# Kernel tuning notes

Hardware: AMD Instinct MI355X
Metric: run time of the kernel (lower is better)

The kernel has to match this reference:

```python
import jax, jax.numpy as jnp
import numpy as np

N = 50000      # nodes
E = 800000     # edges (avg degree 16)
G = 256        # graphs in batch
IN = 128       # in_channels
H = 256        # hidden_channels
L = 4          # num_layers


def setup_inputs() -> dict:
    key = jax.random.key(0)
    ks = jax.random.split(key, 16)
    x = jax.random.normal(ks[0], (N, IN), dtype=jnp.float32)
    edge_index = jax.random.randint(ks[1], (2, E), 0, N, dtype=jnp.int64)
    batch = jnp.sort(jax.random.randint(ks[2], (N,), 0, G, dtype=jnp.int64))
    s_in = 1.0 / np.sqrt(IN)
    s_h = 1.0 / np.sqrt(H)
    return {
        "x": x,
        "edge_index": edge_index,
        "batch": batch,
        "w1_0": jax.random.normal(ks[3], (IN, H), jnp.float32) * s_in,
        "b1_0": jnp.zeros((H,), jnp.float32),
        "w2_0": jax.random.normal(ks[4], (H, H), jnp.float32) * s_h,
        "b2_0": jnp.zeros((H,), jnp.float32),
        "w1s": jax.random.normal(ks[5], (L - 1, H, H), jnp.float32) * s_h,
        "b1s": jnp.zeros((L - 1, H), jnp.float32),
        "w2s": jax.random.normal(ks[6], (L - 1, H, H), jnp.float32) * s_h,
        "b2s": jnp.zeros((L - 1, H), jnp.float32),
    }


def reference(x, edge_index, batch, w1_0, b1_0, w2_0, b2_0, w1s, b1s, w2s, b2s):
    n_nodes = x.shape[0]
    src, dst = edge_index[0], edge_index[1]

    def gin_layer(h, w1, b1, w2, b2):
        # scatter-add neighbor aggregation: out[i] = sum_{(j->i)} h[j]
        agg = jax.ops.segment_sum(h[src], dst, num_segments=n_nodes)
        z = h + agg  # GIN with eps = 0: (1+eps)*x + aggr
        z = jax.nn.relu(z @ w1 + b1) @ w2 + b2  # MLP: Linear-ReLU-Linear
        return jax.nn.relu(z)  # outer F.relu in forward

    h = gin_layer(x, w1_0, b1_0, w2_0, b2_0)
    for i in range(L - 1):  # small fixed layer loop
        h = gin_layer(h, w1s[i], b1s[i], w2s[i], b2s[i])

    # global_add_pool: per-graph segment sum -> [G, H]
    return jax.ops.segment_sum(h, batch, num_segments=G)
```

## Files before the change

kernel.cpp:

```cpp
#include <hip/hip_runtime.h>
#include <hip/hip_bf16.h>

#define NN 50000
#define NE 800000
#define NG 256
#define CIN 128
#define CH 256

typedef unsigned short u16;
typedef unsigned int u32;
typedef __attribute__((ext_vector_type(8))) short short8;
typedef __attribute__((ext_vector_type(8))) unsigned short ushort8;
typedef __attribute__((ext_vector_type(4))) float f32x4;

__device__ __forceinline__ float bf2f(u16 u) { return __uint_as_float(((u32)u) << 16); }
__device__ __forceinline__ u16 f2bf(float f) {
    u32 u = __float_as_uint(f);
    return (u16)((u + 0x7fffu + ((u >> 16) & 1u)) >> 16);
}

__global__ void k_prep(const float* __restrict__ x, u16* __restrict__ xb,
                       const float* __restrict__ w1_0, const float* __restrict__ w2_0,
                       const float* __restrict__ w1s, const float* __restrict__ w2s,
                       u16* __restrict__ Wp, int* __restrict__ deg_fill,
                       float* __restrict__ outf) {
    int t = blockIdx.x * 256 + threadIdx.x;
    if (t < 2 * NN) deg_fill[t] = 0;
    if (t < NG * CH) outf[t] = 0.f;
    if (t < NN * CIN / 4) {
        float4 v = ((const float4*)x)[t];
        ushort4 o; o.x = f2bf(v.x); o.y = f2bf(v.y); o.z = f2bf(v.z); o.w = f2bf(v.w);
        ((ushort4*)xb)[t] = o;
    }
    if (t < CIN * CH + 7 * CH * CH) {
        const float* Wsrc; int rem;
        if (t < CIN * CH) { Wsrc = w1_0; rem = t; }
        else {
            int o = t - CIN * CH;
            int m = o >> 16; rem = o & 65535;
            Wsrc = (m == 0) ? w2_0
                 : (m <= 3) ? w1s + (size_t)(m - 1) * 65536
                            : w2s + (size_t)(m - 4) * 65536;
        }
        int j = rem & 7, lane = (rem >> 3) & 63, nt = (rem >> 9) & 15, kb = rem >> 13;
        int k = kb * 32 + ((lane >> 4) << 3) + j;
        int nc = nt * 16 + (lane & 15);
        Wp[t] = f2bf(Wsrc[k * CH + nc]);
    }
}

__global__ void k_count_deg(const int* __restrict__ dst, int* __restrict__ deg) {
    int e = blockIdx.x * 256 + threadIdx.x;
    if (e < NE) atomicAdd(&deg[dst[e]], 1);
}

__global__ void k_scan1(const int* __restrict__ deg, int* __restrict__ bsum) {
    __shared__ int sd[256];
    int base = blockIdx.x * 1024, t = threadIdx.x, s = 0;
    for (int j = 0; j < 4; j++) { int i = base + t * 4 + j; if (i < NN) s += deg[i]; }
    sd[t] = s; __syncthreads();
    for (int off = 128; off > 0; off >>= 1) { if (t < off) sd[t] += sd[t + off]; __syncthreads(); }
    if (t == 0) bsum[blockIdx.x] = sd[0];
}

__global__ void k_scan2(int* bsum, int nb, int* row_ptr) {
    int lane = threadIdx.x;
    int v = (lane < nb) ? bsum[lane] : 0;
    int s = v;
    for (int off = 1; off < 64; off <<= 1) {
        int t = __shfl_up(s, off, 64);
        if (lane >= off) s += t;
    }
    if (lane < nb) bsum[lane] = s - v;
    if (lane == 0) row_ptr[NN] = NE;
}

__global__ void k_scan3(const int* __restrict__ deg, const int* __restrict__ bsum,
                        int* __restrict__ row_ptr) {
    __shared__ int sd[256];
    int base = blockIdx.x * 1024, t = threadIdx.x;
    int v[4]; int s = 0;
    for (int j = 0; j < 4; j++) { int i = base + t * 4 + j; v[j] = (i < NN) ? deg[i] : 0; s += v[j]; }
    sd[t] = s; __syncthreads();
    for (int off = 1; off < 256; off <<= 1) {
        int tmp = (t >= off) ? sd[t - off] : 0; __syncthreads();
        sd[t] += tmp; __syncthreads();
    }
    int run = bsum[blockIdx.x] + sd[t] - s;
    for (int j = 0; j < 4; j++) { int i = base + t * 4 + j; if (i < NN) row_ptr[i] = run; run += v[j]; }
}

__global__ void k_fill(const int* __restrict__ src, const int* __restrict__ dst,
                       const int* __restrict__ row_ptr, int* __restrict__ fill,
                       int* __restrict__ col) {
    int e = blockIdx.x * 256 + threadIdx.x;
    if (e < NE) {
        int d = dst[e];
        int pos = row_ptr[d] + atomicAdd(&fill[d], 1);
        col[pos] = src[e];
    }
}

#define ZS 264
template <int K1, bool POOL>
__global__ __launch_bounds__(256, 8) void k_layer(const u16* __restrict__ G,
                                                  const int* __restrict__ row_ptr,
                                                  const int* __restrict__ col,
                                                  const u16* __restrict__ Wp1,
                                                  const float* __restrict__ b1,
                                                  const u16* __restrict__ Wp2,
                                                  const float* __restrict__ b2,
                                                  u16* __restrict__ out,
                                                  const int* __restrict__ batchp,
                                                  float* __restrict__ outf) {
    __shared__ __align__(16) u16 zs[32 * ZS];
    const int tid = threadIdx.x;
    const int wave = tid >> 6, lane = tid & 63;
    const int quad = lane >> 4, l16 = lane & 15;
    const int m0 = blockIdx.x * 32;

    constexpr int LPR = K1 / 8;
    constexpr int RPG = 64 / LPR;
    const int sub = lane / LPR;
    const int c0 = (lane % LPR) * 8;
    for (int g = 0; g < 8; g += RPG) {
        int lr = wave * 8 + g + sub;
        int r = m0 + lr; if (r >= NN) r = NN - 1;
        const u16* base = G + c0;
        float a[8];
        ushort8 sv = *(const ushort8*)(base + (size_t)r * K1);
#pragma unroll
        for (int i = 0; i < 8; i++) a[i] = bf2f(sv[i]);
        int beg = row_ptr[r], end = row_ptr[r + 1];
        int e = beg;
        for (; e + 8 <= end; e += 8) {
            ushort8 v[8];
#pragma unroll
            for (int q = 0; q < 8; q++)
                v[q] = *(const ushort8*)(base + (size_t)col[e + q] * K1);
#pragma unroll
            for (int q = 0; q < 8; q++)
#pragma unroll
                for (int i = 0; i < 8; i++) a[i] += bf2f(v[q][i]);
        }
        for (; e < end; e++) {
            ushort8 nv = *(const ushort8*)(base + (size_t)col[e] * K1);
#pragma unroll
            for (int i = 0; i < 8; i++) a[i] += bf2f(nv[i]);
        }
        ushort8 o;
#pragma unroll
        for (int i = 0; i < 8; i++) o[i] = f2bf(a[i]);
        *(ushort8*)(zs + lr * ZS + c0) = o;
    }
    __syncthreads();

    f32x4 acc[2][4];
#pragma unroll
    for (int ri = 0; ri < 2; ri++)
#pragma unroll
        for (int nj = 0; nj < 4; nj++) acc[ri][nj] = (f32x4){0.f, 0.f, 0.f, 0.f};

    const u16* w1b = Wp1 + (wave * 4) * 512 + lane * 8;
    const u16* w2b = Wp2 + (wave * 4) * 512 + lane * 8;
    constexpr int KB1 = K1 / 32;
    short8 b_cur[4], b_nxt[4];
#pragma unroll
    for (int nj = 0; nj < 4; nj++) b_cur[nj] = *(const short8*)(w1b + nj * 512);

#pragma unroll
    for (int kb = 0; kb < KB1; kb++) {
        int kn = (kb + 1 < KB1) ? (kb + 1) : kb;
#pragma unroll
        for (int nj = 0; nj < 4; nj++)
            b_nxt[nj] = *(const short8*)(w1b + kn * 8192 + nj * 512);
        short8 a[2];
#pragma unroll
        for (int ri = 0; ri < 2; ri++)
            a[ri] = *(const short8*)(zs + (ri * 16 + l16) * ZS + kb * 32 + quad * 8);
#pragma unroll
        for (int nj = 0; nj < 4; nj++)
#pragma unroll
            for (int ri = 0; ri < 2; ri++)
                acc[ri][nj] = __builtin_amdgcn_mfma_f32_16x16x32_bf16(a[ri], b_cur[nj], acc[ri][nj], 0, 0, 0);
#pragma unroll
        for (int nj = 0; nj < 4; nj++) b_cur[nj] = b_nxt[nj];
    }

    short8 b2_cur[4];
#pragma unroll
    for (int nj = 0; nj < 4; nj++) b2_cur[nj] = *(const short8*)(w2b + nj * 512);

    __syncthreads();

#pragma unroll
    for (int nj = 0; nj < 4; nj++) {
        int cc = wave * 64 + nj * 16 + l16;
        float bv = b1[cc];
#pragma unroll
        for (int ri = 0; ri < 2; ri++) {
            f32x4 v = acc[ri][nj];
#pragma unroll
            for (int j = 0; j < 4; j++)
                zs[(ri * 16 + quad * 4 + j) * ZS + cc] = f2bf(fmaxf(v[j] + bv, 0.f));
        }
    }
    __syncthreads();

#pragma unroll
    for (int ri = 0; ri < 2; ri++)
#pragma unroll
        for (int nj = 0; nj < 4; nj++) acc[ri][nj] = (f32x4){0.f, 0.f, 0.f, 0.f};

#pragma unroll
    for (int kb = 0; kb < 8; kb++) {
        int kn = (kb + 1 < 8) ? (kb + 1) : kb;
#pragma unroll
        for (int nj = 0; nj < 4; nj++)
            b_nxt[nj] = *(const short8*)(w2b + kn * 8192 + nj * 512);
        short8 a[2];
#pragma unroll
        for (int ri = 0; ri < 2; ri++)
            a[ri] = *(const short8*)(zs + (ri * 16 + l16) * ZS + kb * 32 + quad * 8);
#pragma unroll
        for (int nj = 0; nj < 4; nj++)
#pragma unroll
            for (int ri = 0; ri < 2; ri++)
                acc[ri][nj] = __builtin_amdgcn_mfma_f32_16x16x32_bf16(a[ri], b2_cur[nj], acc[ri][nj], 0, 0, 0);
#pragma unroll
        for (int nj = 0; nj < 4; nj++) b2_cur[nj] = b_nxt[nj];
    }
    __syncthreads();

#pragma unroll
    for (int nj = 0; nj < 4; nj++) {
        int cc = wave * 64 + nj * 16 + l16;
        float bv = b2[cc];
#pragma unroll
        for (int ri = 0; ri < 2; ri++) {
            f32x4 v = acc[ri][nj];
#pragma unroll
            for (int j = 0; j < 4; j++)
                zs[(ri * 16 + quad * 4 + j) * ZS + cc] = f2bf(fmaxf(v[j] + bv, 0.f));
        }
    }
    __syncthreads();

    if (!POOL) {
        int row = tid >> 3, cb = (tid & 7) * 32;
        if (m0 + row < NN) {
            uint4* dst = (uint4*)(out + (size_t)(m0 + row) * CH + cb);
            const u16* srcp = zs + row * ZS + cb;
#pragma unroll
            for (int c = 0; c < 4; c++) dst[c] = *(const uint4*)(srcp + c * 8);
        }
    } else {
        int c = tid;
        float acc2 = 0.f;
        int cur_g = batchp[m0];
        for (int row = 0; row < 32; row++) {
            int r = m0 + row;
            if (r >= NN) break;
            int g = batchp[r];
            if (g != cur_g) {
                atomicAdd(&outf[cur_g * CH + c], acc2);
                acc2 = 0.f; cur_g = g;
            }
            acc2 += bf2f(zs[row * ZS + c]);
        }
        atomicAdd(&outf[cur_g * CH + c], acc2);
    }
}

extern "C" void kernel_launch(void* const* d_in, const int* in_sizes, int n_in,
                              void* d_out, int out_size, void* d_ws, size_t ws_size,
                              hipStream_t stream) {
    const float* x     = (const float*)d_in[0];
    const int*   ei    = (const int*)d_in[1];
    const int*   batch = (const int*)d_in[2];
    const float* w1_0  = (const float*)d_in[3];
    const float* b1_0  = (const float*)d_in[4];
    const float* w2_0  = (const float*)d_in[5];
    const float* b2_0  = (const float*)d_in[6];
    const float* w1s   = (const float*)d_in[7];
    const float* b1s   = (const float*)d_in[8];
    const float* w2s   = (const float*)d_in[9];
    const float* b2s   = (const float*)d_in[10];
    float* out = (float*)d_out;

    char* p = (char*)d_ws;
    u16* Hb  = (u16*)p; p += (size_t)NN * CH * 2;
    u16* Tb  = (u16*)p; p += (size_t)NN * CH * 2;
    u16* xb  = (u16*)p; p += (size_t)NN * CIN * 2;
    u16* WpA = (u16*)p; p += (size_t)(CIN * CH + 7 * CH * CH) * 2;
    int* row_ptr = (int*)p; p += (size_t)(NN + 1) * 4;
    int* deg  = (int*)p; p += (size_t)NN * 4;
    int* fill = (int*)p; p += (size_t)NN * 4;
    int* col  = (int*)p; p += (size_t)NE * 4;
    int* bsum = (int*)p; p += 256 * 4;

    u16* Wp1_0 = WpA;
    u16* Wp2_0 = Wp1_0 + CIN * CH;
    u16* Wp1sA = Wp2_0 + CH * CH;
    u16* Wp2sA = Wp1sA + 3 * CH * CH;

    const int* srcv = ei;
    const int* dstv = ei + NE;

    int nb = (NN + 1023) / 1024;

    hipLaunchKernelGGL(k_prep, dim3((NN * CIN / 4 + 255) / 256), dim3(256), 0, stream,
                       x, xb, w1_0, w2_0, w1s, w2s, WpA, deg, out);

    hipLaunchKernelGGL(k_count_deg, dim3((NE + 255) / 256), dim3(256), 0, stream, dstv, deg);
    hipLaunchKernelGGL(k_scan1, dim3(nb), dim3(256), 0, stream, deg, bsum);
    hipLaunchKernelGGL(k_scan2, dim3(1), dim3(64), 0, stream, bsum, nb, row_ptr);
    hipLaunchKernelGGL(k_scan3, dim3(nb), dim3(256), 0, stream, deg, bsum, row_ptr);
    hipLaunchKernelGGL(k_fill, dim3((NE + 255) / 256), dim3(256), 0, stream, srcv, dstv, row_ptr, fill, col);

    int layerBlocks = (NN + 31) / 32;

    hipLaunchKernelGGL((k_layer<128, false>), dim3(layerBlocks), dim3(256), 0, stream,
                       xb, row_ptr, col, Wp1_0, b1_0, Wp2_0, b2_0, Hb, batch, out);
    hipLaunchKernelGGL((k_layer<256, false>), dim3(layerBlocks), dim3(256), 0, stream,
                       Hb, row_ptr, col, Wp1sA, b1s, Wp2sA, b2s, Tb, batch, out);
    hipLaunchKernelGGL((k_layer<256, false>), dim3(layerBlocks), dim3(256), 0, stream,
                       Tb, row_ptr, col, Wp1sA + (size_t)CH * CH, b1s + CH,
                       Wp2sA + (size_t)CH * CH, b2s + CH, Hb, batch, out);
    hipLaunchKernelGGL((k_layer<256, true>), dim3(layerBlocks), dim3(256), 0, stream,
                       Hb, row_ptr, col, Wp1sA + (size_t)2 * CH * CH, b1s + 2 * CH,
                       Wp2sA + (size_t)2 * CH * CH, b2s + 2 * CH, (u16*)nullptr, batch, out);
}
```

Baseline: 463.7 us.

## Fold block-sum scan into scan3 and shrink gather unroll to four

Removes the separate single-wave scan2 launch by having every scan3 block redundantly compute the exclusive prefix over the 49 block sums in its first wave, and moves the row_ptr[NN] write into scan3. This saves one kernel launch and its dependency gap. Separately, the neighbour-gather loop in the layer kernel now unrolls by 4 instead of 8, which lowers register pressure but leaves fewer loads in flight per thread.

```diff
diff --git a/kernel.cpp b/kernel.cpp
--- a/kernel.cpp
+++ b/kernel.cpp
@@ -54,6 +54,7 @@
     if (e < NE) atomicAdd(&deg[dst[e]], 1);
 }
 
+#define NB 49
 __global__ void k_scan1(const int* __restrict__ deg, int* __restrict__ bsum) {
     __shared__ int sd[256];
     int base = blockIdx.x * 1024, t = threadIdx.x, s = 0;
@@ -63,22 +64,21 @@
     if (t == 0) bsum[blockIdx.x] = sd[0];
 }
 
-__global__ void k_scan2(int* bsum, int nb, int* row_ptr) {
-    int lane = threadIdx.x;
-    int v = (lane < nb) ? bsum[lane] : 0;
-    int s = v;
-    for (int off = 1; off < 64; off <<= 1) {
-        int t = __shfl_up(s, off, 64);
-        if (lane >= off) s += t;
-    }
-    if (lane < nb) bsum[lane] = s - v;
-    if (lane == 0) row_ptr[NN] = NE;
-}
-
 __global__ void k_scan3(const int* __restrict__ deg, const int* __restrict__ bsum,
                         int* __restrict__ row_ptr) {
     __shared__ int sd[256];
-    int base = blockIdx.x * 1024, t = threadIdx.x;
+    __shared__ int sblk[64];
+    int t = threadIdx.x;
+    if (t < 64) {
+        int v = (t < NB) ? bsum[t] : 0;
+        int s = v;
+        for (int off = 1; off < 64; off <<= 1) {
+            int t2 = __shfl_up(s, off, 64);
+            if (t >= off) s += t2;
+        }
+        sblk[t] = s - v;
+    }
+    int base = blockIdx.x * 1024;
     int v[4]; int s = 0;
     for (int j = 0; j < 4; j++) { int i = base + t * 4 + j; v[j] = (i < NN) ? deg[i] : 0; s += v[j]; }
     sd[t] = s; __syncthreads();
@@ -86,8 +86,9 @@
         int tmp = (t >= off) ? sd[t - off] : 0; __syncthreads();
         sd[t] += tmp; __syncthreads();
     }
-    int run = bsum[blockIdx.x] + sd[t] - s;
+    int run = sblk[blockIdx.x] + sd[t] - s;
     for (int j = 0; j < 4; j++) { int i = base + t * 4 + j; if (i < NN) row_ptr[i] = run; run += v[j]; }
+    if (blockIdx.x == 0 && t == 0) row_ptr[NN] = NE;
 }
 
 __global__ void k_fill(const int* __restrict__ src, const int* __restrict__ dst,
@@ -133,15 +134,14 @@
         for (int i = 0; i < 8; i++) a[i] = bf2f(sv[i]);
         int beg = row_ptr[r], end = row_ptr[r + 1];
         int e = beg;
-        for (; e + 8 <= end; e += 8) {
-            ushort8 v[8];
-#pragma unroll
-            for (int q = 0; q < 8; q++)
-                v[q] = *(const ushort8*)(base + (size_t)col[e + q] * K1);
-#pragma unroll
-            for (int q = 0; q < 8; q++)
-#pragma unroll
-                for (int i = 0; i < 8; i++) a[i] += bf2f(v[q][i]);
+        for (; e + 4 <= end; e += 4) {
+            ushort8 v0 = *(const ushort8*)(base + (size_t)col[e] * K1);
+            ushort8 v1 = *(const ushort8*)(base + (size_t)col[e + 1] * K1);
+            ushort8 v2 = *(const ushort8*)(base + (size_t)col[e + 2] * K1);
+            ushort8 v3 = *(const ushort8*)(base + (size_t)col[e + 3] * K1);
+#pragma unroll
+            for (int i = 0; i < 8; i++)
+                a[i] += bf2f(v0[i]) + bf2f(v1[i]) + bf2f(v2[i]) + bf2f(v3[i]);
         }
         for (; e < end; e++) {
             ushort8 nv = *(const ushort8*)(base + (size_t)col[e] * K1);
@@ -307,15 +307,12 @@
     const int* srcv = ei;
     const int* dstv = ei + NE;
 
-    int nb = (NN + 1023) / 1024;
-
     hipLaunchKernelGGL(k_prep, dim3((NN * CIN / 4 + 255) / 256), dim3(256), 0, stream,
                        x, xb, w1_0, w2_0, w1s, w2s, WpA, deg, out);
 
     hipLaunchKernelGGL(k_count_deg, dim3((NE + 255) / 256), dim3(256), 0, stream, dstv, deg);
-    hipLaunchKernelGGL(k_scan1, dim3(nb), dim3(256), 0, stream, deg, bsum);
-    hipLaunchKernelGGL(k_scan2, dim3(1), dim3(64), 0, stream, bsum, nb, row_ptr);
-    hipLaunchKernelGGL(k_scan3, dim3(nb), dim3(256), 0, stream, deg, bsum, row_ptr);
+    hipLaunchKernelGGL(k_scan1, dim3(NB), dim3(256), 0, stream, deg, bsum);
+    hipLaunchKernelGGL(k_scan3, dim3(NB), dim3(256), 0, stream, deg, bsum, row_ptr);
     hipLaunchKernelGGL(k_fill, dim3((NE + 255) / 256), dim3(256), 0, stream, srcv, dstv, row_ptr, fill, col);
 
     int layerBlocks = (NN + 31) / 32;
```

Result: no change. 458.4 us (-1.2%).
